# Kernel tuning notes

Measured on AMD Instinct MI355X. Metric: run time of the kernel, lower is better.

Reference implementation:

```python
import jax, jax.numpy as jnp
import numpy as np

N = 50000          # num_nodes
E = 1600000        # num directed edges
IN_C = 128         # in_channels
OUT_C = 128        # out_channels
HEADS = 8
HFD = OUT_C // HEADS  # head_feat_dim = 16
NEG_SLOPE = 0.2


def setup_inputs() -> dict:
    key = jax.random.key(0)
    k1, k2, k3, k4, k5 = jax.random.split(key, 5)
    node_feats = jax.random.normal(k1, (N, IN_C), dtype=jnp.float32)
    edge_index = jax.random.randint(k2, (2, E), 0, N, dtype=jnp.int64)
    # parameters (xavier-ish scale, kept small so exp() stays in range)
    W = jax.random.normal(k3, (OUT_C, IN_C), dtype=jnp.float32) * (1.0 / np.sqrt(IN_C))
    a_left = jax.random.normal(k4, (HFD, HEADS), dtype=jnp.float32) * 0.1
    a_right = jax.random.normal(k5, (HFD, HEADS), dtype=jnp.float32) * 0.1
    bias = jnp.zeros((OUT_C,), dtype=jnp.float32)
    return {"node_feats": node_feats, "edge_index": edge_index,
            "W": W, "a_left": a_left, "a_right": a_right, "bias": bias}


def reference(node_feats, edge_index, W, a_left, a_right, bias):
    n = node_feats.shape[0]
    # embedding: Linear without bias, then split into heads -> [n, h, c]
    emb = (node_feats @ W.T).reshape(n, HEADS, HFD)
    # per-node attention logit halves: sum_c emb[n,h,c] * a[c,h] -> [n, h]
    left = jnp.einsum('nhc,ch->nh', emb, a_left)
    right = jnp.einsum('nhc,ch->nh', emb, a_right)
    src = edge_index[0]
    dst = edge_index[1]
    # edge logit: score(src, dst) uses a_left on src, a_right on dst
    e = left[src] + right[dst]                       # [E, h]
    e = jnp.where(e >= 0, e, NEG_SLOPE * e)          # leaky relu(0.2)
    w = jnp.exp(e)                                   # [E, h] (module uses raw exp)
    denom = jax.ops.segment_sum(w, dst, num_segments=n)  # [n, h]
    attn = w / denom[dst]                            # [E, h]
    msg = emb[src] * attn[:, :, None]                # [E, h, c]
    out = jax.ops.segment_sum(msg, dst, num_segments=n)  # [n, h, c]
    # concat heads + bias
    out = out.reshape(n, HEADS * HFD) + bias
    return out
```

## Files before the change

### kernel.cpp

```cpp
#include <hip/hip_runtime.h>
#include <hip/hip_bf16.h>

#define N_NODES 50000
#define N_EDGES 1600000
#define HEADS 8
#define HFD 16
#define CH 128

#define PART 128
#define NB 391
#define BCAP 5120
#define PA_T 512
#define PA_CHUNK 3200
#define PA_PER 7
#define PA_BLOCKS 500

#define QPART 32
#define QCAP 1536
#define AG_TASKS (NB * 4)
#define AG_BLOCKS 1568

typedef __bf16 bf16x8 __attribute__((ext_vector_type(8)));
typedef __bf16 bf16x4 __attribute__((ext_vector_type(4)));
typedef float f32x4 __attribute__((ext_vector_type(4)));

__device__ __forceinline__ float bf_lo(unsigned u) { return __uint_as_float(u << 16); }
__device__ __forceinline__ float bf_hi(unsigned u) { return __uint_as_float(u & 0xffff0000u); }

__global__ __launch_bounds__(256) void k_splitw(const float* __restrict__ W,
                                                const float* __restrict__ aL,
                                                const float* __restrict__ aR,
                                                __bf16* __restrict__ Whi,
                                                __bf16* __restrict__ Wlo,
                                                __bf16* __restrict__ Vhi,
                                                __bf16* __restrict__ Vlo,
                                                int* __restrict__ bucket_cnt) {
  int t = blockIdx.x * 256 + threadIdx.x;
  if (t < NB) bucket_cnt[t] = 0;
  if (t < CH * CH / 4) {
    f32x4 v = ((const f32x4*)W)[t];
    bf16x4 h, l;
#pragma unroll
    for (int i = 0; i < 4; ++i) {
      __bf16 hb = (__bf16)v[i];
      h[i] = hb;
      l[i] = (__bf16)(v[i] - (float)hb);
    }
    ((bf16x4*)Whi)[t] = h;
    ((bf16x4*)Wlo)[t] = l;
  }
  if (t < 16 * CH) {
    int j = t >> 7;
    int k = t & 127;
    int h = j & 7;
    const float* a = (j < 8) ? aL : aR;
    float v = 0.f;
#pragma unroll
    for (int c = 0; c < HFD; ++c) v += W[(h * HFD + c) * CH + k] * a[c * HEADS + h];
    __bf16 hb = (__bf16)v;
    Vhi[t] = hb;
    Vlo[t] = (__bf16)(v - (float)hb);
  }
}

__global__ __launch_bounds__(64) void k_emb(const float* __restrict__ X,
                                            const __bf16* __restrict__ Whi,
                                            const __bf16* __restrict__ Wlo,
                                            const __bf16* __restrict__ Vhi,
                                            const __bf16* __restrict__ Vlo,
                                            __bf16* __restrict__ embb,
                                            float* __restrict__ leftp,
                                            float* __restrict__ rightp) {
  int ntile = blockIdx.x;
  int lane = threadIdx.x;
  int c = lane & 15, quad = lane >> 4;
  const float* xp = X + (size_t)(ntile * 16 + c) * CH + quad * 8;
  bf16x8 xh[4], xl[4];
#pragma unroll
  for (int ks = 0; ks < 4; ++ks) {
    float4 x0 = *(const float4*)(xp + ks * 32);
    float4 x1 = *(const float4*)(xp + ks * 32 + 4);
    float xv[8] = {x0.x, x0.y, x0.z, x0.w, x1.x, x1.y, x1.z, x1.w};
#pragma unroll
    for (int j = 0; j < 8; ++j) {
      __bf16 hb = (__bf16)xv[j];
      xh[ks][j] = hb;
      xl[ks][j] = (__bf16)(xv[j] - (float)hb);
    }
  }
#pragma unroll
  for (int h = 0; h < HEADS; ++h) {
    const __bf16* wp = Whi + (size_t)(h * 16 + c) * CH + quad * 8;
    const __bf16* wlp = Wlo + (size_t)(h * 16 + c) * CH + quad * 8;
    f32x4 acc = {0.f, 0.f, 0.f, 0.f};
#pragma unroll
    for (int ks = 0; ks < 4; ++ks) {
      bf16x8 wh = *(const bf16x8*)(wp + ks * 32);
      bf16x8 wl = *(const bf16x8*)(wlp + ks * 32);
      acc = __builtin_amdgcn_mfma_f32_16x16x32_bf16(xl[ks], wh, acc, 0, 0, 0);
      acc = __builtin_amdgcn_mfma_f32_16x16x32_bf16(xh[ks], wl, acc, 0, 0, 0);
      acc = __builtin_amdgcn_mfma_f32_16x16x32_bf16(xh[ks], wh, acc, 0, 0, 0);
    }
#pragma unroll
    for (int r = 0; r < 4; ++r) {
      int node = ntile * 16 + quad * 4 + r;
      embb[(size_t)node * CH + h * HFD + c] = (__bf16)acc[r];
    }
  }
  {
    const __bf16* vp = Vhi + (size_t)c * CH + quad * 8;
    const __bf16* vlp = Vlo + (size_t)c * CH + quad * 8;
    f32x4 acc = {0.f, 0.f, 0.f, 0.f};
#pragma unroll
    for (int ks = 0; ks < 4; ++ks) {
      bf16x8 vh = *(const bf16x8*)(vp + ks * 32);
      bf16x8 vl = *(const bf16x8*)(vlp + ks * 32);
      acc = __builtin_amdgcn_mfma_f32_16x16x32_bf16(xl[ks], vh, acc, 0, 0, 0);
      acc = __builtin_amdgcn_mfma_f32_16x16x32_bf16(xh[ks], vl, acc, 0, 0, 0);
      acc = __builtin_amdgcn_mfma_f32_16x16x32_bf16(xh[ks], vh, acc, 0, 0, 0);
    }
#pragma unroll
    for (int r = 0; r < 4; ++r) {
      int node = ntile * 16 + quad * 4 + r;
      if (c < 8) leftp[node * HEADS + c] = acc[r];
      else rightp[node * HEADS + (c - 8)] = acc[r];
    }
  }
}

__global__ __launch_bounds__(PA_T) void k_bucket(const int* __restrict__ ei,
                                                 int* __restrict__ bucket_cnt,
                                                 unsigned* __restrict__ ebuf) {
  __shared__ unsigned sp[PA_CHUNK];
  __shared__ int hist[NB];
  __shared__ int lcur[NB];
  __shared__ int wbase[NB];
  __shared__ int scn[PA_T];
  int t = threadIdx.x;
  int base = blockIdx.x * PA_CHUNK;
  for (int i = t; i < NB; i += PA_T) hist[i] = 0;
  __syncthreads();
  unsigned pk[PA_PER];
#pragma unroll
  for (int i = 0; i < PA_PER; ++i) {
    int e = t + i * PA_T;
    pk[i] = 0xffffffffu;
    if (e < PA_CHUNK) {
      int src = ei[base + e];
      int dst = ei[N_EDGES + base + e];
      pk[i] = ((unsigned)(dst >> 7) << 23) | ((unsigned)(dst & 127) << 16) |
              (unsigned)src;
      atomicAdd(&hist[dst >> 7], 1);
    }
  }
  __syncthreads();
  scn[t] = (t < NB) ? hist[t] : 0;
  __syncthreads();
  int val = scn[t];
  for (int d = 1; d < PA_T; d <<= 1) {
    int o = (t >= d) ? scn[t - d] : 0;
    __syncthreads();
    val += o;
    scn[t] = val;
    __syncthreads();
  }
  if (t < NB) {
    int hv = hist[t];
    int lstart = val - hv;
    lcur[t] = lstart;
    int prior = hv ? atomicAdd(&bucket_cnt[t], hv) : 0;
    wbase[t] = t * BCAP + prior - lstart;
  }
  __syncthreads();
#pragma unroll
  for (int i = 0; i < PA_PER; ++i) {
    if (pk[i] != 0xffffffffu) {
      int b = pk[i] >> 23;
      int pos = atomicAdd(&lcur[b], 1);
      sp[pos] = pk[i];
    }
  }
  __syncthreads();
  for (int i = t; i < PA_CHUNK; i += PA_T) {
    unsigned p = sp[i];
    int b = p >> 23;
    int slot = wbase[b] + i;
    if (slot < (b + 1) * BCAP) ebuf[slot] = p;
  }
}

__global__ __launch_bounds__(256) void k_aggr(const int* __restrict__ bucket_cnt,
                                              const unsigned* __restrict__ ebuf,
                                              const __bf16* __restrict__ embb,
                                              const float* __restrict__ leftp,
                                              const float* __restrict__ rightp,
                                              const float* __restrict__ bias,
                                              float* __restrict__ out) {
  __shared__ unsigned short su[QCAP];
  __shared__ int hist[QPART];
  __shared__ int pfx[QPART];
  __shared__ int cur[QPART];
  int T = (blockIdx.x & 7) * (AG_BLOCKS / 8) + (blockIdx.x >> 3);
  if (T >= AG_TASKS) return;
  int b = T >> 2;
  int q = T & 3;
  int t = threadIdx.x;
  int cnt = bucket_cnt[b];
  if (cnt > BCAP) cnt = BCAP;
  int ebase = b * BCAP;
  if (t < QPART) hist[t] = 0;
  __syncthreads();
  for (int e4 = t * 4; e4 < cnt; e4 += 1024) {
    uint4 pp = *(const uint4*)(ebuf + ebase + e4);
    unsigned pj[4] = {pp.x, pp.y, pp.z, pp.w};
#pragma unroll
    for (int j = 0; j < 4; ++j) {
      if (e4 + j < cnt) {
        int dl = (pj[j] >> 16) & 127;
        if ((dl >> 5) == q) atomicAdd(&hist[dl & 31], 1);
      }
    }
  }
  __syncthreads();
  if (t < 64) {
    int v = (t < QPART) ? hist[t] : 0;
#pragma unroll
    for (int d = 1; d < QPART; d <<= 1) {
      int o = __shfl_up(v, d);
      if (t >= d) v += o;
    }
    if (t < QPART) {
      int ex = v - hist[t];
      pfx[t] = ex;
      cur[t] = ex;
    }
  }
  __syncthreads();
  for (int e4 = t * 4; e4 < cnt; e4 += 1024) {
    uint4 pp = *(const uint4*)(ebuf + ebase + e4);
    unsigned pj[4] = {pp.x, pp.y, pp.z, pp.w};
#pragma unroll
    for (int j = 0; j < 4; ++j) {
      if (e4 + j < cnt) {
        unsigned p = pj[j];
        int dl = (p >> 16) & 127;
        if ((dl >> 5) == q) {
          int pos = atomicAdd(&cur[dl & 31], 1);
          if (pos < QCAP) su[pos] = (unsigned short)(p & 0xffffu);
        }
      }
    }
  }
  __syncthreads();

  int wv = t >> 6;
  int lane = t & 63;
  int g = lane >> 4;
  int m = lane & 15;
  int h = m >> 1;
#pragma unroll 1
  for (int k = 0; k < 8; ++k) {
    int dl = wv * 8 + k;
    int dst = b * PART + q * QPART + dl;
    bool valid = dst < N_NODES;
    int beg = pfx[dl];
    int cd = hist[dl];
    if (beg + cd > QCAP) cd = QCAP - beg;
    float r = valid ? rightp[dst * HEADS + h] : 0.f;
    float acc[8] = {0.f, 0.f, 0.f, 0.f, 0.f, 0.f, 0.f, 0.f};
    float dsum = 0.f;
    if (cd > 0) {
      int sA0, sA1, sB0, sB1;
      uint4 uA0, uA1, uB0, uB1;
      float lA0, lA1, lB0, lB1;
#define STAGE(E0, s0, s1, u0, u1, l0, l1)                          \
      {                                                            \
        int i0 = (E0) + g, i1 = (E0) + 4 + g;                      \
        s0 = su[beg + ((i0 < cd) ? i0 : 0)];                       \
        s1 = su[beg + ((i1 < cd) ? i1 : 0)];                       \
        u0 = ((const uint4*)(embb + (size_t)s0 * CH))[m];          \
        u1 = ((const uint4*)(embb + (size_t)s1 * CH))[m];          \
        l0 = leftp[s0 * HEADS + h];                                \
        l1 = leftp[s1 * HEADS + h];                                \
      }
#define CONSUME(E0, u0, u1, l0, l1)                                \
      {                                                            \
        bool a0 = (E0) + g < cd, a1 = (E0) + 4 + g < cd;           \
        float x0 = l0 + r;                                         \
        x0 = (x0 >= 0.f) ? x0 : 0.2f * x0;                         \
        float w0 = a0 ? __expf(x0) : 0.f;                          \
        float x1 = l1 + r;                                         \
        x1 = (x1 >= 0.f) ? x1 : 0.2f * x1;                         \
        float w1 = a1 ? __expf(x1) : 0.f;                          \
        dsum += w0 + w1;                                           \
        acc[0] += w0 * bf_lo(u0.x) + w1 * bf_lo(u1.x);             \
        acc[1] += w0 * bf_hi(u0.x) + w1 * bf_hi(u1.x);             \
        acc[2] += w0 * bf_lo(u0.y) + w1 * bf_lo(u1.y);             \
        acc[3] += w0 * bf_hi(u0.y) + w1 * bf_hi(u1.y);             \
        acc[4] += w0 * bf_lo(u0.z) + w1 * bf_lo(u1.z);             \
        acc[5] += w0 * bf_hi(u0.z) + w1 * bf_hi(u1.z);             \
        acc[6] += w0 * bf_lo(u0.w) + w1 * bf_lo(u1.w);             \
        acc[7] += w0 * bf_hi(u0.w) + w1 * bf_hi(u1.w);             \
      }
      STAGE(0, sA0, sA1, uA0, uA1, lA0, lA1);
      int e0 = 0;
      while (true) {
        if (e0 + 8 < cd) STAGE(e0 + 8, sB0, sB1, uB0, uB1, lB0, lB1);
        CONSUME(e0, uA0, uA1, lA0, lA1);
        e0 += 8;
        if (e0 >= cd) break;
        if (e0 + 8 < cd) STAGE(e0 + 8, sA0, sA1, uA0, uA1, lA0, lA1);
        CONSUME(e0, uB0, uB1, lB0, lB1);
        e0 += 8;
        if (e0 >= cd) break;
      }
#undef STAGE
#undef CONSUME
    }
#pragma unroll
    for (int mask = 16; mask <= 32; mask <<= 1) {
      dsum += __shfl_xor(dsum, mask);
#pragma unroll
      for (int j = 0; j < 8; ++j) acc[j] += __shfl_xor(acc[j], mask);
    }
    if (g == 0 && valid) {
      float inv = (dsum > 0.f) ? 1.0f / dsum : 0.f;
      float4 b0 = ((const float4*)bias)[2 * m];
      float4 b1 = ((const float4*)bias)[2 * m + 1];
      float4 o0 = {acc[0] * inv + b0.x, acc[1] * inv + b0.y,
                   acc[2] * inv + b0.z, acc[3] * inv + b0.w};
      float4 o1 = {acc[4] * inv + b1.x, acc[5] * inv + b1.y,
                   acc[6] * inv + b1.z, acc[7] * inv + b1.w};
      ((float4*)(out + (size_t)dst * CH))[2 * m] = o0;
      ((float4*)(out + (size_t)dst * CH))[2 * m + 1] = o1;
    }
  }
}

extern "C" void kernel_launch(void* const* d_in, const int* in_sizes, int n_in,
                              void* d_out, int out_size, void* d_ws, size_t ws_size,
                              hipStream_t stream) {
  const float* X = (const float*)d_in[0];
  const int* ei = (const int*)d_in[1];
  const float* W = (const float*)d_in[2];
  const float* al = (const float*)d_in[3];
  const float* ar = (const float*)d_in[4];
  const float* bias = (const float*)d_in[5];
  float* out = (float*)d_out;

  unsigned* ebuf = (unsigned*)d_ws;
  __bf16* embb = (__bf16*)(ebuf + (size_t)NB * BCAP);
  __bf16* Whi = embb + (size_t)N_NODES * CH;
  __bf16* Wlo = Whi + CH * CH;
  __bf16* Vhi = Wlo + CH * CH;
  __bf16* Vlo = Vhi + 16 * CH;
  float* leftp = (float*)(Vlo + 16 * CH);
  float* rightp = leftp + (size_t)N_NODES * HEADS;
  int* bucket_cnt = (int*)(rightp + (size_t)N_NODES * HEADS);

  k_splitw<<<16, 256, 0, stream>>>(W, al, ar, Whi, Wlo, Vhi, Vlo, bucket_cnt);
  k_bucket<<<PA_BLOCKS, PA_T, 0, stream>>>(ei, bucket_cnt, ebuf);
  k_emb<<<N_NODES / 16, 64, 0, stream>>>(X, Whi, Wlo, Vhi, Vlo, embb, leftp, rightp);
  k_aggr<<<AG_BLOCKS, 256, 0, stream>>>(bucket_cnt, ebuf, embb, leftp, rightp, bias, out);
}
```

Measured before the change: 204.1 us.

## Use wave-shuffle scan in bucketing, triple-buffer gathers, pack FMAs

The bucketing kernel's shared-memory Hillis-Steele scan, which needed many barriers, is replaced by a wavefront shuffle scan plus a small cross-wave combine. The aggregation loop moves from double to triple buffering of the gathered source embeddings and logits, so more loads are in flight per wave. The accumulators become float2 vectors so the compiler can issue packed FMA instructions. Together these are meant to cut barrier overhead, hide gather latency and reduce ALU instruction count, at the cost of higher register pressure that could lower occupancy.

```diff
diff --git a/kernel.cpp b/kernel.cpp
--- a/kernel.cpp
+++ b/kernel.cpp
@@ -23,6 +23,7 @@
 typedef __bf16 bf16x8 __attribute__((ext_vector_type(8)));
 typedef __bf16 bf16x4 __attribute__((ext_vector_type(4)));
 typedef float f32x4 __attribute__((ext_vector_type(4)));
+typedef float f32x2 __attribute__((ext_vector_type(2)));
 
 __device__ __forceinline__ float bf_lo(unsigned u) { return __uint_as_float(u << 16); }
 __device__ __forceinline__ float bf_hi(unsigned u) { return __uint_as_float(u & 0xffff0000u); }
@@ -135,7 +136,7 @@
   __shared__ int hist[NB];
   __shared__ int lcur[NB];
   __shared__ int wbase[NB];
-  __shared__ int scn[PA_T];
+  __shared__ int wpart[8];
   int t = threadIdx.x;
   int base = blockIdx.x * PA_CHUNK;
   for (int i = t; i < NB; i += PA_T) hist[i] = 0;
@@ -154,18 +155,28 @@
     }
   }
   __syncthreads();
-  scn[t] = (t < NB) ? hist[t] : 0;
-  __syncthreads();
-  int val = scn[t];
-  for (int d = 1; d < PA_T; d <<= 1) {
-    int o = (t >= d) ? scn[t - d] : 0;
-    __syncthreads();
-    val += o;
-    scn[t] = val;
-    __syncthreads();
-  }
+  int hv = (t < NB) ? hist[t] : 0;
+  int lane = t & 63, wid = t >> 6;
+  int v = hv;
+#pragma unroll
+  for (int d = 1; d < 64; d <<= 1) {
+    int o = __shfl_up(v, d);
+    if (lane >= d) v += o;
+  }
+  if (lane == 63) wpart[wid] = v;
+  __syncthreads();
+  if (t < 8) {
+    int pv = wpart[t];
+#pragma unroll
+    for (int d = 1; d < 8; d <<= 1) {
+      int o = __shfl_up(pv, d);
+      if (t >= d) pv += o;
+    }
+    wpart[t] = pv;
+  }
+  __syncthreads();
+  int val = v + ((wid > 0) ? wpart[wid - 1] : 0);
   if (t < NB) {
-    int hv = hist[t];
     int lstart = val - hv;
     lcur[t] = lstart;
     int prior = hv ? atomicAdd(&bucket_cnt[t], hv) : 0;
@@ -267,12 +278,16 @@
     int cd = hist[dl];
     if (beg + cd > QCAP) cd = QCAP - beg;
     float r = valid ? rightp[dst * HEADS + h] : 0.f;
-    float acc[8] = {0.f, 0.f, 0.f, 0.f, 0.f, 0.f, 0.f, 0.f};
+    f32x2 acc2[4];
+    acc2[0] = (f32x2){0.f, 0.f};
+    acc2[1] = (f32x2){0.f, 0.f};
+    acc2[2] = (f32x2){0.f, 0.f};
+    acc2[3] = (f32x2){0.f, 0.f};
     float dsum = 0.f;
     if (cd > 0) {
-      int sA0, sA1, sB0, sB1;
-      uint4 uA0, uA1, uB0, uB1;
-      float lA0, lA1, lB0, lB1;
+      int sA0, sA1, sB0, sB1, sC0, sC1;
+      uint4 uA0, uA1, uB0, uB1, uC0, uC1;
+      float lA0, lA1, lB0, lB1, lC0, lC1;
 #define STAGE(E0, s0, s1, u0, u1, l0, l1)                          \
       {                                                            \
         int i0 = (E0) + g, i1 = (E0) + 4 + g;                      \
@@ -293,44 +308,58 @@
         x1 = (x1 >= 0.f) ? x1 : 0.2f * x1;                         \
         float w1 = a1 ? __expf(x1) : 0.f;                          \
         dsum += w0 + w1;                                           \
-        acc[0] += w0 * bf_lo(u0.x) + w1 * bf_lo(u1.x);             \
-        acc[1] += w0 * bf_hi(u0.x) + w1 * bf_hi(u1.x);             \
-        acc[2] += w0 * bf_lo(u0.y) + w1 * bf_lo(u1.y);             \
-        acc[3] += w0 * bf_hi(u0.y) + w1 * bf_hi(u1.y);             \
-        acc[4] += w0 * bf_lo(u0.z) + w1 * bf_lo(u1.z);             \
-        acc[5] += w0 * bf_hi(u0.z) + w1 * bf_hi(u1.z);             \
-        acc[6] += w0 * bf_lo(u0.w) + w1 * bf_lo(u1.w);             \
-        acc[7] += w0 * bf_hi(u0.w) + w1 * bf_hi(u1.w);             \
+        f32x2 wv0 = {w0, w0}, wv1 = {w1, w1};                      \
+        acc2[0] += wv0 * (f32x2){bf_lo(u0.x), bf_hi(u0.x)}         \
+                 + wv1 * (f32x2){bf_lo(u1.x), bf_hi(u1.x)};        \
+        acc2[1] += wv0 * (f32x2){bf_lo(u0.y), bf_hi(u0.y)}         \
+                 + wv1 * (f32x2){bf_lo(u1.y), bf_hi(u1.y)};        \
+        acc2[2] += wv0 * (f32x2){bf_lo(u0.z), bf_hi(u0.z)}         \
+                 + wv1 * (f32x2){bf_lo(u1.z), bf_hi(u1.z)};        \
+        acc2[3] += wv0 * (f32x2){bf_lo(u0.w), bf_hi(u0.w)}         \
+                 + wv1 * (f32x2){bf_lo(u1.w), bf_hi(u1.w)};        \
       }
       STAGE(0, sA0, sA1, uA0, uA1, lA0, lA1);
+      if (8 < cd) STAGE(8, sB0, sB1, uB0, uB1, lB0, lB1);
       int e0 = 0;
       while (true) {
-        if (e0 + 8 < cd) STAGE(e0 + 8, sB0, sB1, uB0, uB1, lB0, lB1);
+        if (e0 + 16 < cd) STAGE(e0 + 16, sC0, sC1, uC0, uC1, lC0, lC1);
         CONSUME(e0, uA0, uA1, lA0, lA1);
         e0 += 8;
         if (e0 >= cd) break;
-        if (e0 + 8 < cd) STAGE(e0 + 8, sA0, sA1, uA0, uA1, lA0, lA1);
+        if (e0 + 16 < cd) STAGE(e0 + 16, sA0, sA1, uA0, uA1, lA0, lA1);
         CONSUME(e0, uB0, uB1, lB0, lB1);
         e0 += 8;
         if (e0 >= cd) break;
+        if (e0 + 16 < cd) STAGE(e0 + 16, sB0, sB1, uB0, uB1, lB0, lB1);
+        CONSUME(e0, uC0, uC1, lC0, lC1);
+        e0 += 8;
+        if (e0 >= cd) break;
       }
 #undef STAGE
 #undef CONSUME
     }
+    float a0 = acc2[0].x, a1 = acc2[0].y, a2 = acc2[1].x, a3 = acc2[1].y;
+    float a4 = acc2[2].x, a5 = acc2[2].y, a6 = acc2[3].x, a7 = acc2[3].y;
 #pragma unroll
     for (int mask = 16; mask <= 32; mask <<= 1) {
       dsum += __shfl_xor(dsum, mask);
-#pragma unroll
-      for (int j = 0; j < 8; ++j) acc[j] += __shfl_xor(acc[j], mask);
+      a0 += __shfl_xor(a0, mask);
+      a1 += __shfl_xor(a1, mask);
+      a2 += __shfl_xor(a2, mask);
+      a3 += __shfl_xor(a3, mask);
+      a4 += __shfl_xor(a4, mask);
+      a5 += __shfl_xor(a5, mask);
+      a6 += __shfl_xor(a6, mask);
+      a7 += __shfl_xor(a7, mask);
     }
     if (g == 0 && valid) {
       float inv = (dsum > 0.f) ? 1.0f / dsum : 0.f;
       float4 b0 = ((const float4*)bias)[2 * m];
       float4 b1 = ((const float4*)bias)[2 * m + 1];
-      float4 o0 = {acc[0] * inv + b0.x, acc[1] * inv + b0.y,
-                   acc[2] * inv + b0.z, acc[3] * inv + b0.w};
-      float4 o1 = {acc[4] * inv + b1.x, acc[5] * inv + b1.y,
-                   acc[6] * inv + b1.z, acc[7] * inv + b1.w};
+      float4 o0 = {a0 * inv + b0.x, a1 * inv + b0.y,
+                   a2 * inv + b0.z, a3 * inv + b0.w};
+      float4 o1 = {a4 * inv + b1.x, a5 * inv + b1.y,
+                   a6 * inv + b1.z, a7 * inv + b1.w};
       ((float4*)(out + (size_t)dst * CH))[2 * m] = o0;
       ((float4*)(out + (size_t)dst * CH))[2 * m + 1] = o1;
     }
```

Result: no change. 203.7 us (-0.2%).
